# Performance work log

Measured on AMD Instinct MI355X. Metric: run time of the kernel, lower is better.

The kernel has to match this reference:

```python
import jax, jax.numpy as jnp
import numpy as np

NODE_DIM = 256
EDGE_DIM = 128
NODE_IN = 768 + 769 + 4 + 1 + 3  # 1545


def setup_inputs() -> dict:
    key = jax.random.key(0)
    ks = jax.random.split(key, 16)
    B, N, H, W, C = 8, 128, 128, 128, 768
    obj_feats = jax.random.normal(ks[0], (B, N, 769), dtype=jnp.float32)
    masks = jax.random.uniform(ks[1], (B, N, H, W), dtype=jnp.float32)
    features = jax.random.normal(ks[2], (B, C, H, W), dtype=jnp.float32)
    bboxes = jax.random.uniform(ks[3], (B, N, 4), dtype=jnp.float32)
    conf = jax.random.uniform(ks[4], (B, N), dtype=jnp.float32)
    depth = jax.random.uniform(ks[5], (B, 1, H, W), dtype=jnp.float32) + 0.1
    # near-identity pose so homogeneous divide is well-conditioned
    pose = jnp.eye(4, dtype=jnp.float32)[None] + 0.01 * jax.random.normal(ks[6], (B, 4, 4), dtype=jnp.float32)
    s = 0.02
    node_w1 = s * jax.random.normal(ks[7], (512, NODE_IN), dtype=jnp.float32)
    node_b1 = jnp.zeros((512,), dtype=jnp.float32)
    node_w2 = s * jax.random.normal(ks[8], (NODE_DIM, 512), dtype=jnp.float32)
    node_b2 = jnp.zeros((NODE_DIM,), dtype=jnp.float32)
    edge_w1 = s * jax.random.normal(ks[9], (256, 2 * NODE_DIM), dtype=jnp.float32)
    edge_b1 = jnp.zeros((256,), dtype=jnp.float32)
    edge_w2 = s * jax.random.normal(ks[10], (EDGE_DIM, 256), dtype=jnp.float32)
    edge_b2 = jnp.zeros((EDGE_DIM,), dtype=jnp.float32)
    return dict(obj_feats=obj_feats, masks=masks, features=features, bboxes=bboxes,
                conf=conf, depth=depth, pose=pose,
                node_w1=node_w1, node_b1=node_b1, node_w2=node_w2, node_b2=node_b2,
                edge_w1=edge_w1, edge_b1=edge_b1, edge_w2=edge_w2, edge_b2=edge_b2)


def _forward(obj_feats, masks, features, bboxes, conf, depth, pose,
             node_w1, node_b1, node_w2, node_b2,
             edge_w1, edge_b1, edge_w2, edge_b2):
    B, C, H, W = features.shape
    N = masks.shape[1]
    K = jnp.eye(3, dtype=features.dtype)  # self.intrinsics

    # --- mask pooling: normalized mask-weighted average of features ---
    feats_flat = features.reshape(B, C, H * W)                 # [B,C,HW]
    m_flat = masks.reshape(B, N, H * W)                        # [B,N,HW]
    m_norm = m_flat / (m_flat.sum(-1, keepdims=True) + 1e-6)
    pooled = jnp.einsum('bnh,bch->bnc', m_norm, feats_flat)    # [B,N,C]

    # --- positional encoding ---
    x1, y1, x2, y2 = bboxes[..., 0], bboxes[..., 1], bboxes[..., 2], bboxes[..., 3]
    pos_feat = jnp.stack([(x1 + x2) / 2, (y1 + y2) / 2, x2 - x1, y2 - y1], axis=-1)  # [B,N,4]

    # --- motion prior ---
    ys = jnp.arange(H, dtype=masks.dtype)
    xs = jnp.arange(W, dtype=masks.dtype)
    mask_sum = masks.sum((-1, -2)) + 1e-6                      # [B,N]
    cx = jnp.einsum('bnhw,w->bn', masks, xs) / mask_sum
    cy = jnp.einsum('bnhw,h->bn', masks, ys) / mask_sum
    cx_idx = jnp.clip(jnp.round(cx).astype(jnp.int32), 0, W - 1)
    cy_idx = jnp.clip(jnp.round(cy).astype(jnp.int32), 0, H - 1)
    b_idx = jnp.arange(B)[:, None]                             # [B,1]
    z = depth[b_idx, 0, cy_idx, cx_idx]                        # [B,N]
    X = (cx - K[0, 2]) * z / K[0, 0]
    Y = (cy - K[1, 2]) * z / K[1, 1]
    ones = jnp.ones_like(z)
    P_h = jnp.stack([X, Y, z, ones], axis=-1)                  # [B,N,4]
    P_next = jnp.einsum('bij,bnj->bni', pose, P_h)             # [B,N,4]
    motion = P_next[..., :3] / P_next[..., 3:]                 # [B,N,3]

    # --- node MLP ---
    node_input = jnp.concatenate([pooled, obj_feats, pos_feat, conf[..., None], motion], axis=-1)
    h = jax.nn.relu(node_input @ node_w1.T + node_b1)
    node_emb = h @ node_w2.T + node_b2                         # [B,N,node_dim]

    # --- edge MLP: cat([n_i, n_j]) @ W1 == n_i @ W1a + n_j @ W1b (avoid O(N^2 * 2D) cat) ---
    D = node_emb.shape[-1]
    w1a, w1b = edge_w1[:, :D], edge_w1[:, D:]
    hi = node_emb @ w1a.T                                      # [B,N,256]
    hj = node_emb @ w1b.T                                      # [B,N,256]
    he = jax.nn.relu(hi[:, :, None, :] + hj[:, None, :, :] + edge_b1)  # [B,N,N,256]
    edge_emb = he @ edge_w2.T + edge_b2                        # [B,N,N,edge_dim]

    # --- adjacency: exp(-cdist) ---
    sq = jnp.sum(node_emb * node_emb, axis=-1)                 # [B,N]
    d2 = sq[:, :, None] + sq[:, None, :] - 2.0 * jnp.einsum('bnd,bmd->bnm', node_emb, node_emb)
    d2 = jnp.maximum(d2, 0.0)
    d = jnp.where(d2 > 0, jnp.sqrt(jnp.where(d2 > 0, d2, 1.0)), 0.0)  # grad-safe sqrt at 0
    adj = jnp.exp(-d)
    return node_emb, edge_emb, adj


def reference(obj_feats, masks, features, bboxes, conf, depth, pose,
              node_w1, node_b1, node_w2, node_b2,
              edge_w1, edge_b1, edge_w2, edge_b2):
    return _forward(obj_feats, masks, features, bboxes, conf, depth, pose,
                    node_w1, node_b1, node_w2, node_b2,
                    edge_w1, edge_b1, edge_w2, edge_b2)
```

## Files before the change

### kernel.cpp

```cpp
#include <hip/hip_runtime.h>
#include <hip/hip_bf16.h>

#define B_   8
#define N_   128
#define HW_  16384
#define C_   768
#define NIN_ 1545
#define NINP_ 1600
#define D1_  512
#define D_   256
#define EO_  128
#define KC_  16

typedef short s16x8 __attribute__((ext_vector_type(8)));
typedef float f32x16 __attribute__((ext_vector_type(16)));

__device__ __forceinline__ unsigned short f2bf(float x) {
  union { __hip_bfloat16 h; unsigned short u; } cv;
  cv.h = __float2bfloat16(x);
  return cv.u;
}

__global__ __launch_bounds__(256) void prep_k(const float* __restrict__ masks,
                                              const float* __restrict__ depth,
                                              const float* __restrict__ pose,
                                              float4* __restrict__ stats,
                                              const float* __restrict__ w1,
                                              const float* __restrict__ w2,
                                              const float* __restrict__ ew1,
                                              const float* __restrict__ ew2,
                                              unsigned short* __restrict__ w1b,
                                              unsigned short* __restrict__ w2b,
                                              unsigned short* __restrict__ we1b,
                                              unsigned short* __restrict__ ew2b) {
  if (blockIdx.x >= 1024) {
    int i = (blockIdx.x - 1024) * 256 + threadIdx.x;
    if (i < 512 * NINP_) {
      int r = i / NINP_, k = i - r * NINP_;
      w1b[i] = f2bf(k < NIN_ ? w1[r * NIN_ + k] : 0.0f);
      return;
    }
    i -= 512 * NINP_;
    if (i < 256 * 512) { w2b[i] = f2bf(w2[i]); return; }
    i -= 256 * 512;
    if (i < 512 * 256) {
      int r = i >> 8, k = i & 255;
      we1b[i] = f2bf(r < 256 ? ew1[r * 512 + k] : ew1[(r - 256) * 512 + 256 + k]);
      return;
    }
    i -= 512 * 256;
    if (i < 128 * 256) { ew2b[i] = f2bf(ew2[i]); }
    return;
  }
  int row = blockIdx.x;
  int b = row >> 7;
  const float4* mp = (const float4*)(masks + (size_t)row * HW_);
  double s = 0.0, sx = 0.0, sy = 0.0;
  for (int it = 0; it < 16; ++it) {
    int i4 = threadIdx.x + it * 256;
    float4 v = mp[i4];
    int flat = i4 * 4;
    int y = flat >> 7, xb = flat & 127;
    double rs = (double)v.x + (double)v.y + (double)v.z + (double)v.w;
    s += rs;
    sx += (double)v.x * xb + (double)v.y * (xb + 1) + (double)v.z * (xb + 2) + (double)v.w * (xb + 3);
    sy += rs * (double)y;
  }
  for (int off = 32; off; off >>= 1) {
    s  += __shfl_down(s,  off);
    sx += __shfl_down(sx, off);
    sy += __shfl_down(sy, off);
  }
  __shared__ double red[3][4];
  int w = threadIdx.x >> 6, l = threadIdx.x & 63;
  if (l == 0) { red[0][w] = s; red[1][w] = sx; red[2][w] = sy; }
  __syncthreads();
  if (threadIdx.x == 0) {
    s  = red[0][0] + red[0][1] + red[0][2] + red[0][3];
    sx = red[1][0] + red[1][1] + red[1][2] + red[1][3];
    sy = red[2][0] + red[2][1] + red[2][2] + red[2][3];
    double msum = s + 1e-6;
    double cx = sx / msum, cy = sy / msum;
    int cxi = (int)rint(cx); cxi = min(127, max(0, cxi));
    int cyi = (int)rint(cy); cyi = min(127, max(0, cyi));
    double z = (double)depth[(size_t)b * HW_ + cyi * 128 + cxi];
    double Ph[4] = { cx * z, cy * z, z, 1.0 };
    const float* P = pose + b * 16;
    double pn[4];
    #pragma unroll
    for (int r = 0; r < 4; ++r)
      pn[r] = (double)P[r*4+0]*Ph[0] + (double)P[r*4+1]*Ph[1] + (double)P[r*4+2]*Ph[2] + (double)P[r*4+3]*Ph[3];
    double inv3 = 1.0 / pn[3];
    stats[row] = make_float4((float)(1.0 / msum), (float)(pn[0]*inv3), (float)(pn[1]*inv3), (float)(pn[2]*inv3));
  }
}

__global__ __launch_bounds__(256) void pooled_k(const float* __restrict__ masks,
                                                const float* __restrict__ feats,
                                                float* __restrict__ Spart) {
  __shared__ short As[128 * 72];
  __shared__ short Bs[128 * 72];
  int id = blockIdx.x + 96 * blockIdx.y;
  int lg = (id & 7) * 96 + (id >> 3);
  int b  = lg / 96;
  int lx = lg - b * 96;
  int ct = lx % 6, kc = lx / 6;
  const float* mb = masks + (size_t)b * N_ * HW_;
  const float* fb = feats + ((size_t)b * C_ + (size_t)ct * 128) * HW_;
  int t = threadIdx.x, w = t >> 6, l = t & 63;
  int rsel = l & 31, khalf = l >> 5;
  f32x16 acc[4];
  #pragma unroll
  for (int nt = 0; nt < 4; ++nt)
    #pragma unroll
    for (int i = 0; i < 16; ++i) acc[nt][i] = 0.0f;

  for (int kt = 0; kt < 16; ++kt) {
    int kbase = kc * 1024 + kt * 64;
    #pragma unroll
    for (int c = 0; c < 8; ++c) {
      int chunk = t + 256 * c;
      int row = chunk >> 4;
      int kof = (chunk & 15) << 2;
      float4 va = *(const float4*)(mb + (size_t)row * HW_ + kbase + kof);
      ushort4 pa = { f2bf(va.x), f2bf(va.y), f2bf(va.z), f2bf(va.w) };
      *(ushort4*)((unsigned short*)As + row * 72 + kof) = pa;
      float4 vb = *(const float4*)(fb + (size_t)row * HW_ + kbase + kof);
      ushort4 pb = { f2bf(vb.x), f2bf(vb.y), f2bf(vb.z), f2bf(vb.w) };
      *(ushort4*)((unsigned short*)Bs + row * 72 + kof) = pb;
    }
    __syncthreads();
    #pragma unroll
    for (int ks = 0; ks < 4; ++ks) {
      s16x8 a = *(const s16x8*)&As[(w * 32 + rsel) * 72 + ks * 16 + khalf * 8];
      #pragma unroll
      for (int nt = 0; nt < 4; ++nt) {
        s16x8 bf = *(const s16x8*)&Bs[(nt * 32 + rsel) * 72 + ks * 16 + khalf * 8];
        acc[nt] = __builtin_amdgcn_mfma_f32_32x32x16_bf16(a, bf, acc[nt], 0, 0, 0);
      }
    }
    __syncthreads();
  }
  float* op = Spart + (size_t)kc * 786432 + (size_t)b * 98304;
  #pragma unroll
  for (int nt = 0; nt < 4; ++nt)
    #pragma unroll
    for (int reg = 0; reg < 16; ++reg) {
      int rm = w * 32 + (reg & 3) + 8 * (reg >> 2) + 4 * khalf;
      int cn = ct * 128 + nt * 32 + rsel;
      op[rm * C_ + cn] = acc[nt][reg];
    }
}

__global__ __launch_bounds__(256) void assemble_k(const float* __restrict__ Spart,
                                                  const float4* __restrict__ stats,
                                                  const float* __restrict__ obj,
                                                  const float* __restrict__ bboxes,
                                                  const float* __restrict__ conf,
                                                  unsigned short* __restrict__ ni) {
  int r = blockIdx.x;
  float4 st = stats[r];
  float x1 = bboxes[r*4+0], y1 = bboxes[r*4+1], x2 = bboxes[r*4+2], y2 = bboxes[r*4+3];
  for (int k = threadIdx.x; k < NINP_; k += 256) {
    float v;
    if (k < 768) {
      float acc = 0.0f;
      #pragma unroll
      for (int kc = 0; kc < KC_; ++kc) acc += Spart[(size_t)kc * 786432 + (size_t)r * C_ + k];
      v = acc * st.x;
    } else if (k < 1537) v = obj[(size_t)r * 769 + (k - 768)];
    else if (k == 1537) v = 0.5f * (x1 + x2);
    else if (k == 1538) v = 0.5f * (y1 + y2);
    else if (k == 1539) v = x2 - x1;
    else if (k == 1540) v = y2 - y1;
    else if (k == 1541) v = conf[r];
    else if (k == 1542) v = st.y;
    else if (k == 1543) v = st.z;
    else if (k == 1544) v = st.w;
    else v = 0.0f;
    ni[(size_t)r * NINP_ + k] = f2bf(v);
  }
}

template <bool RELU, bool BIAS, int OUTM>
__global__ __launch_bounds__(256) void gemm64_k(const unsigned short* __restrict__ A,
                                                const unsigned short* __restrict__ Bm,
                                                const float* __restrict__ bias,
                                                float* __restrict__ Cf,
                                                unsigned short* __restrict__ Cb,
                                                int K, int N) {
  __shared__ short As[64 * 72];
  __shared__ short Bs[64 * 72];
  int n0 = blockIdx.x * 64, m0 = blockIdx.y * 64;
  int t = threadIdx.x, w = t >> 6, l = t & 63;
  int rsel = l & 31, khalf = l >> 5;
  int mh = (w & 1) * 32, nh = (w >> 1) * 32;
  f32x16 acc;
  #pragma unroll
  for (int i = 0; i < 16; ++i) acc[i] = 0.0f;

  for (int k0 = 0; k0 < K; k0 += 64) {
    #pragma unroll
    for (int c = 0; c < 2; ++c) {
      int chunk = t + 256 * c;
      int row = chunk >> 3, kof = (chunk & 7) * 8;
      *(uint4*)((unsigned short*)As + row * 72 + kof) =
          *(const uint4*)&A[(size_t)(m0 + row) * K + k0 + kof];
      *(uint4*)((unsigned short*)Bs + row * 72 + kof) =
          *(const uint4*)&Bm[(size_t)(n0 + row) * K + k0 + kof];
    }
    __syncthreads();
    #pragma unroll
    for (int ks = 0; ks < 4; ++ks) {
      s16x8 a = *(const s16x8*)&As[(mh + rsel) * 72 + ks * 16 + khalf * 8];
      s16x8 bf = *(const s16x8*)&Bs[(nh + rsel) * 72 + ks * 16 + khalf * 8];
      acc = __builtin_amdgcn_mfma_f32_32x32x16_bf16(a, bf, acc, 0, 0, 0);
    }
    __syncthreads();
  }
  #pragma unroll
  for (int reg = 0; reg < 16; ++reg) {
    int rm = m0 + mh + (reg & 3) + 8 * (reg >> 2) + 4 * khalf;
    int cn = n0 + nh + rsel;
    float v = acc[reg];
    if (BIAS) v += bias[cn];
    if (RELU) v = fmaxf(v, 0.0f);
    if (OUTM == 0 || OUTM == 2) Cf[(size_t)rm * N + cn] = v;
    if (OUTM == 1 || OUTM == 2) Cb[(size_t)rm * N + cn] = f2bf(v);
  }
}

__global__ __launch_bounds__(256) void edge_adj_k(const float* __restrict__ hihj,
                                                  const unsigned short* __restrict__ ew2b,
                                                  const float* __restrict__ eb1,
                                                  const float* __restrict__ eb2,
                                                  const float* __restrict__ ne,
                                                  float* __restrict__ out_edge,
                                                  float* __restrict__ out_adj) {
  __shared__ union {
    struct { short W2s[128 * 264]; float hi_s[256]; float b1_s[256]; float b2_s[128]; } e;
    struct { float njs[128 * 65]; float nei[256]; float red[3][256]; } a;
  } sm;
  int id = blockIdx.x;
  int lg = (id & 7) * 256 + (id >> 3);
  int t = threadIdx.x;

  if (lg < 1024) {
    int bi = lg;
    int b = bi >> 7;
    int w = t >> 6, l = t & 63;
    int rsel = l & 31, khalf = l >> 5;

    #pragma unroll
    for (int c = 0; c < 16; ++c) {
      int chunk = t + 256 * c;
      int row = chunk >> 5, kof = (chunk & 31) * 8;
      *(uint4*)((unsigned short*)sm.e.W2s + row * 264 + kof) = *(const uint4*)&ew2b[row * 256 + kof];
    }
    sm.e.hi_s[t] = hihj[(size_t)bi * 512 + t];
    sm.e.b1_s[t] = eb1[t];
    if (t < 128) sm.e.b2_s[t] = eb2[t];
    __syncthreads();

    f32x16 acc[4];
    #pragma unroll
    for (int nt = 0; nt < 4; ++nt)
      #pragma unroll
      for (int i = 0; i < 16; ++i) acc[nt][i] = 0.0f;

    const float* hjb = hihj + (size_t)b * 128 * 512 + 256;
    int jrow = w * 32 + rsel;
    #pragma unroll
    for (int ks = 0; ks < 16; ++ks) {
      int k0 = ks * 16 + khalf * 8;
      const float* hp = hjb + (size_t)jrow * 512 + k0;
      float4 h0 = *(const float4*)hp;
      float4 h1 = *(const float4*)(hp + 4);
      float f[8] = { h0.x, h0.y, h0.z, h0.w, h1.x, h1.y, h1.z, h1.w };
      s16x8 a;
      #pragma unroll
      for (int c = 0; c < 8; ++c)
        a[c] = (short)f2bf(fmaxf(f[c] + sm.e.hi_s[k0 + c] + sm.e.b1_s[k0 + c], 0.0f));
      #pragma unroll
      for (int nt = 0; nt < 4; ++nt) {
        s16x8 bf = *(const s16x8*)&sm.e.W2s[(nt * 32 + rsel) * 264 + k0];
        acc[nt] = __builtin_amdgcn_mfma_f32_32x32x16_bf16(a, bf, acc[nt], 0, 0, 0);
      }
    }
    float* ob = out_edge + (size_t)bi * 128 * 128;
    #pragma unroll
    for (int nt = 0; nt < 4; ++nt)
      #pragma unroll
      for (int reg = 0; reg < 16; ++reg) {
        int j = w * 32 + (reg & 3) + 8 * (reg >> 2) + 4 * khalf;
        int o = nt * 32 + rsel;
        ob[(size_t)j * 128 + o] = acc[nt][reg] + sm.e.b2_s[o];
      }
  } else {
    int bi = lg - 1024;
    int b = bi >> 7;
    const float* neb = ne + (size_t)b * 128 * 256;
    int j = t & 127, kh = t >> 7;
    sm.a.nei[t] = ne[(size_t)bi * 256 + t];
    float dot = 0.0f, sqj = 0.0f, sqi = 0.0f;
    for (int tile = 0; tile < 4; ++tile) {
      __syncthreads();
      #pragma unroll
      for (int p = 0; p < 8; ++p) {
        int f = p * 256 + t;
        int row = f >> 4;
        int k4 = (f & 15) << 2;
        float4 v = *(const float4*)(neb + (size_t)row * 256 + tile * 64 + k4);
        float* dst = &sm.a.njs[row * 65 + k4];
        dst[0] = v.x; dst[1] = v.y; dst[2] = v.z; dst[3] = v.w;
      }
      __syncthreads();
      int kb = tile * 64 + kh * 32;
      #pragma unroll
      for (int k = 0; k < 32; ++k) {
        float c = sm.a.njs[j * 65 + kh * 32 + k];
        float aa = sm.a.nei[kb + k];
        dot += aa * c; sqj += c * c; sqi += aa * aa;
      }
    }
    __syncthreads();
    sm.a.red[0][t] = dot; sm.a.red[1][t] = sqj; sm.a.red[2][t] = sqi;
    __syncthreads();
    if (t < 128) {
      dot = sm.a.red[0][t] + sm.a.red[0][t + 128];
      sqj = sm.a.red[1][t] + sm.a.red[1][t + 128];
      sqi = sm.a.red[2][t] + sm.a.red[2][t + 128];
      float d2 = fmaxf(sqi + sqj - 2.0f * dot, 0.0f);
      float d = d2 > 0.0f ? sqrtf(d2) : 0.0f;
      out_adj[(size_t)bi * 128 + t] = expf(-d);
    }
  }
}

extern "C" void kernel_launch(void* const* d_in, const int* in_sizes, int n_in,
                              void* d_out, int out_size, void* d_ws, size_t ws_size,
                              hipStream_t stream) {
  const float* obj    = (const float*)d_in[0];
  const float* masks  = (const float*)d_in[1];
  const float* feats  = (const float*)d_in[2];
  const float* bboxes = (const float*)d_in[3];
  const float* conf   = (const float*)d_in[4];
  const float* depth  = (const float*)d_in[5];
  const float* pose   = (const float*)d_in[6];
  const float* nw1    = (const float*)d_in[7];
  const float* nb1    = (const float*)d_in[8];
  const float* nw2    = (const float*)d_in[9];
  const float* nb2    = (const float*)d_in[10];
  const float* ew1    = (const float*)d_in[11];
  const float* eb1    = (const float*)d_in[12];
  const float* ew2    = (const float*)d_in[13];
  const float* eb2    = (const float*)d_in[14];

  char* ws = (char*)d_ws;
  float*          Spart = (float*)ws;
  unsigned short* h_bf  = (unsigned short*)ws;
  unsigned short* ne_bf = (unsigned short*)(ws + 1048576);
  float*          hihj  = (float*)(ws + 1572864);
  float4*         stats = (float4*)(ws + 50331648);
  unsigned short* ni_bf = (unsigned short*)(ws + 50348032);
  unsigned short* w1b   = (unsigned short*)(ws + 53624832);
  unsigned short* w2b   = (unsigned short*)(ws + 55263232);
  unsigned short* we1b  = (unsigned short*)(ws + 55525376);
  unsigned short* ew2b  = (unsigned short*)(ws + 55787520);

  float* out      = (float*)d_out;
  float* out_ne   = out;
  float* out_edge = out + 262144;
  float* out_adj  = out + 262144 + 16777216;

  prep_k<<<dim3(5376), dim3(256), 0, stream>>>(masks, depth, pose, stats,
                                               nw1, nw2, ew1, ew2, w1b, w2b, we1b, ew2b);
  pooled_k<<<dim3(96, 8), dim3(256), 0, stream>>>(masks, feats, Spart);
  assemble_k<<<dim3(1024), dim3(256), 0, stream>>>(Spart, stats, obj, bboxes, conf, ni_bf);
  gemm64_k<true,  true,  1><<<dim3(8, 16), dim3(256), 0, stream>>>(ni_bf, w1b, nb1, nullptr, h_bf, NINP_, 512);
  gemm64_k<false, true,  2><<<dim3(4, 16), dim3(256), 0, stream>>>(h_bf, w2b, nb2, out_ne, ne_bf, 512, 256);
  gemm64_k<false, false, 0><<<dim3(8, 16), dim3(256), 0, stream>>>(ne_bf, we1b, nullptr, hihj, nullptr, 256, 512);
  edge_adj_k<<<dim3(2048), dim3(256), 0, stream>>>(hihj, ew2b, eb1, eb2, out_ne, out_edge, out_adj);
}
```

Measured before the change: 738.1 us.

## Pre-convert masks to bf16 in prep and retile pooled GEMM

The prep kernel, which already streams the fp32 masks for statistics, now also writes a bf16 copy of them. The pooling GEMM loads that copy directly with 16-byte loads instead of converting fp32 masks in every tile. The pooling tile shrinks to 64 channels per block with 8 K-splits instead of 16, and block ordering now keeps all channel tiles of one batch and K-chunk adjacent. This halves the partial-sum buffer and removes repeated mask conversion. In exchange it adds a 32 MB bf16 write and doubles how many times each mask is re-read.

```diff
diff --git a/kernel.cpp b/kernel.cpp
--- a/kernel.cpp
+++ b/kernel.cpp
@@ -10,7 +10,8 @@
 #define D1_  512
 #define D_   256
 #define EO_  128
-#define KC_  16
+#define KC_  8
+#define CT_  12
 
 typedef short s16x8 __attribute__((ext_vector_type(8)));
 typedef float f32x16 __attribute__((ext_vector_type(16)));
@@ -25,6 +26,7 @@
                                               const float* __restrict__ depth,
                                               const float* __restrict__ pose,
                                               float4* __restrict__ stats,
+                                              unsigned short* __restrict__ masks_bf,
                                               const float* __restrict__ w1,
                                               const float* __restrict__ w2,
                                               const float* __restrict__ ew1,
@@ -55,10 +57,13 @@
   int row = blockIdx.x;
   int b = row >> 7;
   const float4* mp = (const float4*)(masks + (size_t)row * HW_);
+  unsigned short* mo = masks_bf + (size_t)row * HW_;
   double s = 0.0, sx = 0.0, sy = 0.0;
   for (int it = 0; it < 16; ++it) {
     int i4 = threadIdx.x + it * 256;
     float4 v = mp[i4];
+    ushort4 pv = { f2bf(v.x), f2bf(v.y), f2bf(v.z), f2bf(v.w) };
+    *(ushort4*)(mo + i4 * 4) = pv;
     int flat = i4 * 4;
     int y = flat >> 7, xb = flat & 127;
     double rs = (double)v.x + (double)v.y + (double)v.z + (double)v.w;
@@ -95,36 +100,40 @@
   }
 }
 
-__global__ __launch_bounds__(256) void pooled_k(const float* __restrict__ masks,
+__global__ __launch_bounds__(256) void pooled_k(const unsigned short* __restrict__ masks_bf,
                                                 const float* __restrict__ feats,
                                                 float* __restrict__ Spart) {
   __shared__ short As[128 * 72];
-  __shared__ short Bs[128 * 72];
-  int id = blockIdx.x + 96 * blockIdx.y;
-  int lg = (id & 7) * 96 + (id >> 3);
-  int b  = lg / 96;
-  int lx = lg - b * 96;
-  int ct = lx % 6, kc = lx / 6;
-  const float* mb = masks + (size_t)b * N_ * HW_;
-  const float* fb = feats + ((size_t)b * C_ + (size_t)ct * 128) * HW_;
+  __shared__ short Bs[64 * 72];
+  int id = blockIdx.x;
+  int b  = id / 96;
+  int lx = id - b * 96;
+  int ct = lx % 12, kc = lx / 12;
+  const unsigned short* mb = masks_bf + (size_t)b * N_ * HW_;
+  const float* fb = feats + ((size_t)b * C_ + (size_t)ct * 64) * HW_;
   int t = threadIdx.x, w = t >> 6, l = t & 63;
   int rsel = l & 31, khalf = l >> 5;
-  f32x16 acc[4];
+  f32x16 acc[2];
   #pragma unroll
-  for (int nt = 0; nt < 4; ++nt)
+  for (int nt = 0; nt < 2; ++nt)
     #pragma unroll
     for (int i = 0; i < 16; ++i) acc[nt][i] = 0.0f;
 
-  for (int kt = 0; kt < 16; ++kt) {
-    int kbase = kc * 1024 + kt * 64;
-    #pragma unroll
-    for (int c = 0; c < 8; ++c) {
+  for (int kt = 0; kt < 32; ++kt) {
+    int kbase = kc * 2048 + kt * 64;
+    #pragma unroll
+    for (int c = 0; c < 4; ++c) {
+      int chunk = t + 256 * c;
+      int row = chunk >> 3;
+      int kof = (chunk & 7) * 8;
+      *(uint4*)((unsigned short*)As + row * 72 + kof) =
+          *(const uint4*)(mb + (size_t)row * HW_ + kbase + kof);
+    }
+    #pragma unroll
+    for (int c = 0; c < 4; ++c) {
       int chunk = t + 256 * c;
       int row = chunk >> 4;
       int kof = (chunk & 15) << 2;
-      float4 va = *(const float4*)(mb + (size_t)row * HW_ + kbase + kof);
-      ushort4 pa = { f2bf(va.x), f2bf(va.y), f2bf(va.z), f2bf(va.w) };
-      *(ushort4*)((unsigned short*)As + row * 72 + kof) = pa;
       float4 vb = *(const float4*)(fb + (size_t)row * HW_ + kbase + kof);
       ushort4 pb = { f2bf(vb.x), f2bf(vb.y), f2bf(vb.z), f2bf(vb.w) };
       *(ushort4*)((unsigned short*)Bs + row * 72 + kof) = pb;
@@ -134,7 +143,7 @@
     for (int ks = 0; ks < 4; ++ks) {
       s16x8 a = *(const s16x8*)&As[(w * 32 + rsel) * 72 + ks * 16 + khalf * 8];
       #pragma unroll
-      for (int nt = 0; nt < 4; ++nt) {
+      for (int nt = 0; nt < 2; ++nt) {
         s16x8 bf = *(const s16x8*)&Bs[(nt * 32 + rsel) * 72 + ks * 16 + khalf * 8];
         acc[nt] = __builtin_amdgcn_mfma_f32_32x32x16_bf16(a, bf, acc[nt], 0, 0, 0);
       }
@@ -143,11 +152,11 @@
   }
   float* op = Spart + (size_t)kc * 786432 + (size_t)b * 98304;
   #pragma unroll
-  for (int nt = 0; nt < 4; ++nt)
+  for (int nt = 0; nt < 2; ++nt)
     #pragma unroll
     for (int reg = 0; reg < 16; ++reg) {
       int rm = w * 32 + (reg & 3) + 8 * (reg >> 2) + 4 * khalf;
-      int cn = ct * 128 + nt * 32 + rsel;
+      int cn = ct * 64 + nt * 32 + rsel;
       op[rm * C_ + cn] = acc[nt][reg];
     }
 }
@@ -361,21 +370,22 @@
   unsigned short* h_bf  = (unsigned short*)ws;
   unsigned short* ne_bf = (unsigned short*)(ws + 1048576);
   float*          hihj  = (float*)(ws + 1572864);
-  float4*         stats = (float4*)(ws + 50331648);
-  unsigned short* ni_bf = (unsigned short*)(ws + 50348032);
-  unsigned short* w1b   = (unsigned short*)(ws + 53624832);
-  unsigned short* w2b   = (unsigned short*)(ws + 55263232);
-  unsigned short* we1b  = (unsigned short*)(ws + 55525376);
-  unsigned short* ew2b  = (unsigned short*)(ws + 55787520);
+  float4*         stats = (float4*)(ws + 25165824);
+  unsigned short* ni_bf = (unsigned short*)(ws + 25182208);
+  unsigned short* w1b   = (unsigned short*)(ws + 28459008);
+  unsigned short* w2b   = (unsigned short*)(ws + 30097408);
+  unsigned short* we1b  = (unsigned short*)(ws + 30359552);
+  unsigned short* ew2b  = (unsigned short*)(ws + 30621696);
+  unsigned short* mkbf  = (unsigned short*)(ws + 30687232);
 
   float* out      = (float*)d_out;
   float* out_ne   = out;
   float* out_edge = out + 262144;
   float* out_adj  = out + 262144 + 16777216;
 
-  prep_k<<<dim3(5376), dim3(256), 0, stream>>>(masks, depth, pose, stats,
+  prep_k<<<dim3(5376), dim3(256), 0, stream>>>(masks, depth, pose, stats, mkbf,
                                                nw1, nw2, ew1, ew2, w1b, w2b, we1b, ew2b);
-  pooled_k<<<dim3(96, 8), dim3(256), 0, stream>>>(masks, feats, Spart);
+  pooled_k<<<dim3(768), dim3(256), 0, stream>>>(mkbf, feats, Spart);
   assemble_k<<<dim3(1024), dim3(256), 0, stream>>>(Spart, stats, obj, bboxes, conf, ni_bf);
   gemm64_k<true,  true,  1><<<dim3(8, 16), dim3(256), 0, stream>>>(ni_bf, w1b, nb1, nullptr, h_bf, NINP_, 512);
   gemm64_k<false, true,  2><<<dim3(4, 16), dim3(256), 0, stream>>>(h_bf, w2b, nb2, out_ne, ne_bf, 512, 256);
```

After: 735.5 us. About the same (-0.3%).
